# Kernel optimization log

Measured on AMD Instinct MI355X. Metric: run time of the kernel, lower is better.

The kernel has to match this reference:

```python
import jax, jax.numpy as jnp
import numpy as np

B = 8192
I = 1024
H = 1024


def _xavier(key, out_dim, in_dim):
    limit = float(np.sqrt(6.0 / (in_dim + out_dim)))
    return jax.random.uniform(key, (out_dim, in_dim), jnp.float32, -limit, limit)


def setup_inputs() -> dict:
    key = jax.random.key(0)
    ks = jax.random.split(key, 16)
    inp = {
        "x": jax.random.normal(ks[0], (B, I), jnp.float32),
        "h_prev": jax.random.normal(ks[1], (B, H), jnp.float32),
        "c_prev": jax.random.normal(ks[2], (B, H), jnp.float32),
        # input->hidden weights (hidden_size, input_size), hidden->hidden (hidden_size, hidden_size)
        "Wxi": _xavier(ks[3], H, I), "Whi": _xavier(ks[4], H, H),
        "Wxf": _xavier(ks[5], H, I), "Whf": _xavier(ks[6], H, H),
        "Wxc": _xavier(ks[7], H, I), "Whc": _xavier(ks[8], H, H),
        "Wxo": _xavier(ks[9], H, I), "Who": _xavier(ks[10], H, H),
        "bxi": jnp.zeros((H,), jnp.float32), "bhi": jnp.zeros((H,), jnp.float32),
        # forget-gate biases initialized to ones per _init_weights
        "bxf": jnp.ones((H,), jnp.float32), "bhf": jnp.ones((H,), jnp.float32),
        "bxc": jnp.zeros((H,), jnp.float32), "bhc": jnp.zeros((H,), jnp.float32),
        "bxo": jnp.zeros((H,), jnp.float32), "bho": jnp.zeros((H,), jnp.float32),
    }
    return inp


def reference(x, h_prev, c_prev,
              Wxi, Whi, Wxf, Whf, Wxc, Whc, Wxo, Who,
              bxi, bhi, bxf, bhf, bxc, bhc, bxo, bho):
    # Fuse the 8 small linears into two GEMMs: stack along the output (gate) axis.
    Wx = jnp.concatenate([Wxi, Wxf, Wxc, Wxo], axis=0)   # (4H, I)
    Wh = jnp.concatenate([Whi, Whf, Whc, Who], axis=0)   # (4H, H)
    bx = jnp.concatenate([bxi, bxf, bxc, bxo], axis=0)    # (4H,)
    bh = jnp.concatenate([bhi, bhf, bhc, bho], axis=0)    # (4H,)
    gates = x @ Wx.T + h_prev @ Wh.T + (bx + bh)           # (B, 4H)
    zi, zf, zc, zo = jnp.split(gates, 4, axis=1)
    i = jax.nn.sigmoid(zi)
    f = jax.nn.sigmoid(zf)
    g = jnp.tanh(zc)
    o = jax.nn.sigmoid(zo)
    c_new = f * c_prev + i * g
    h_new = o * jnp.tanh(c_new)
    return (h_new, c_new)
```

## Files before the change

kernel.cpp:

```cpp
#include <hip/hip_runtime.h>
#include <hip/hip_bf16.h>
#include <stdint.h>


#define B_DIM 8192
#define I_DIM 1024
#define H_DIM 1024
#define K_DIM 2048
#define N_DIM 4096
#define NKT   32

typedef short bf16x8 __attribute__((ext_vector_type(8)));
typedef float f32x4 __attribute__((ext_vector_type(4)));

__device__ __forceinline__ unsigned short f2bf(float f) {
  unsigned int u = __float_as_uint(f);
  u += 0x7FFFu + ((u >> 16) & 1u);
  return (unsigned short)(u >> 16);
}

__global__ void pack_A_kernel(const float* __restrict__ x,
                              const float* __restrict__ h,
                              unsigned short* __restrict__ outA) {
  const int total = B_DIM * K_DIM / 8;
  for (int idx = blockIdx.x * blockDim.x + threadIdx.x; idx < total;
       idx += gridDim.x * blockDim.x) {
    int row = idx >> 8;
    int col = (idx & 255) * 8;
    const float* src = (col < I_DIM) ? (x + (size_t)row * I_DIM + col)
                                     : (h + (size_t)row * H_DIM + (col - I_DIM));
    const float4* s4 = (const float4*)src;
    float4 v0 = s4[0], v1 = s4[1];
    bf16x8 o;
    o[0] = f2bf(v0.x); o[1] = f2bf(v0.y); o[2] = f2bf(v0.z); o[3] = f2bf(v0.w);
    o[4] = f2bf(v1.x); o[5] = f2bf(v1.y); o[6] = f2bf(v1.z); o[7] = f2bf(v1.w);
    *(bf16x8*)(outA + (size_t)idx * 8) = o;
  }
}

__global__ void pack_B_kernel(const float* __restrict__ Wxi, const float* __restrict__ Whi,
                              const float* __restrict__ Wxf, const float* __restrict__ Whf,
                              const float* __restrict__ Wxc, const float* __restrict__ Whc,
                              const float* __restrict__ Wxo, const float* __restrict__ Who,
                              unsigned short* __restrict__ outB) {
  const int total = N_DIM * K_DIM / 8;
  for (int idx = blockIdx.x * blockDim.x + threadIdx.x; idx < total;
       idx += gridDim.x * blockDim.x) {
    int r = idx >> 8;
    int k = (idx & 255) * 8;
    int g = (r >> 4) & 3;
    int h = ((r >> 6) << 4) | (r & 15);
    const float* base;
    if (k < I_DIM) {
      base = (g == 0) ? Wxi : (g == 1) ? Wxf : (g == 2) ? Wxc : Wxo;
      base += (size_t)h * I_DIM + k;
    } else {
      base = (g == 0) ? Whi : (g == 1) ? Whf : (g == 2) ? Whc : Who;
      base += (size_t)h * H_DIM + (k - I_DIM);
    }
    const float4* s4 = (const float4*)base;
    float4 v0 = s4[0], v1 = s4[1];
    bf16x8 o;
    o[0] = f2bf(v0.x); o[1] = f2bf(v0.y); o[2] = f2bf(v0.z); o[3] = f2bf(v0.w);
    o[4] = f2bf(v1.x); o[5] = f2bf(v1.y); o[6] = f2bf(v1.z); o[7] = f2bf(v1.w);
    *(bf16x8*)(outB + (size_t)idx * 8) = o;
  }
}


#define STAGE(gptr, slotoff, ktile) do {                                          \
    int _ktc = (ktile) < NKT ? (ktile) : (NKT - 1);                               \
    const unsigned short* _g = (gptr) + (size_t)_ktc * 64;                        \
    __builtin_amdgcn_global_load_lds(                                             \
        (const __attribute__((address_space(1))) void*)_g,                        \
        (__attribute__((address_space(3))) void*)(lds + (slotoff) + wid * 1024),  \
        16, 0, 0);                                                                \
    __builtin_amdgcn_global_load_lds(                                             \
        (const __attribute__((address_space(1))) void*)(_g + (size_t)64 * K_DIM), \
        (__attribute__((address_space(3))) void*)(lds + (slotoff) + 8192 + wid * 1024), \
        16, 0, 0);                                                                \
  } while (0)

#define MFMAQ(Q, AR)                                                              \
  _Pragma("unroll") for (int mq = 0; mq < 2; ++mq)                                \
  _Pragma("unroll") for (int nn = 0; nn < 4; ++nn)                                \
  _Pragma("unroll") for (int kk = 0; kk < 2; ++kk)                                \
    acc[(Q)*2 + mq][nn] = __builtin_amdgcn_mfma_f32_16x16x32_bf16(                \
        AR[mq][kk], Bf[nn][kk], acc[(Q)*2 + mq][nn], 0, 0, 0)

#define RD_A(DST, Q)                                                              \
  _Pragma("unroll") for (int mq = 0; mq < 2; ++mq) {                              \
    DST[mq][0] = *(const bf16x8*)(ldsAr + _bo + (Q) * 4096 + mq * 2048 + rd0);    \
    DST[mq][1] = *(const bf16x8*)(ldsAr + _bo + (Q) * 4096 + mq * 2048 + rd1); }

#define KTILE(BUF, KT) do {                                                       \
    const int _bo = (BUF) * 32768;                                                \
    const int _bo1 = ((BUF) ^ 1) * 32768;                                         \
         \
    _Pragma("unroll") for (int nn = 0; nn < 4; ++nn) {                            \
      Bf[nn][0] = *(const bf16x8*)(ldsBr + _bo + nn * 2048 + rd0);                \
      Bf[nn][1] = *(const bf16x8*)(ldsBr + _bo + nn * 2048 + rd1); }              \
    RD_A(AX, 0);                                                                  \
    RD_A(AY, 1);                                                                  \
    STAGE(gA0p, _bo1, (KT) + 1);                                                  \
    __builtin_amdgcn_s_barrier();                                                 \
    __builtin_amdgcn_s_setprio(1);                                                \
    MFMAQ(0, AX);                                                                 \
    __builtin_amdgcn_s_setprio(0);                                                \
    __builtin_amdgcn_s_barrier();                                                 \
          \
    RD_A(AX, 2);                                                                  \
    STAGE(gA1p, _bo1 + 16384, (KT) + 1);                                          \
    __builtin_amdgcn_s_barrier();                                                 \
    __builtin_amdgcn_s_setprio(1);                                                \
    MFMAQ(1, AY);                                                                 \
    __builtin_amdgcn_s_setprio(0);                                                \
    __builtin_amdgcn_s_barrier();                                                 \
        \
    RD_A(AY, 3);                                                                  \
    STAGE(gB0p, 65536 + _bo, (KT) + 2);                                           \
    __builtin_amdgcn_s_barrier();                                                 \
    __builtin_amdgcn_s_setprio(1);                                                \
    MFMAQ(2, AX);                                                                 \
    __builtin_amdgcn_s_setprio(0);                                                \
    __builtin_amdgcn_s_barrier();                                                 \
                                                   \
    STAGE(gB1p, 65536 + _bo + 16384, (KT) + 2);                                   \
    __builtin_amdgcn_s_barrier();                                                 \
    __builtin_amdgcn_s_setprio(1);                                                \
    MFMAQ(3, AY);                                                                 \
    __builtin_amdgcn_s_setprio(0);                                                \
    asm volatile("s_waitcnt vmcnt(4)" ::: "memory");                              \
    __builtin_amdgcn_s_barrier();                                                 \
  } while (0)

__launch_bounds__(512, 2)
__global__ void lstm_gemm_kernel(const unsigned short* __restrict__ A,
                                 const unsigned short* __restrict__ Bp,
                                 const float* __restrict__ c_prev,
                                 const float* __restrict__ bxi, const float* __restrict__ bhi,
                                 const float* __restrict__ bxf, const float* __restrict__ bhf,
                                 const float* __restrict__ bxc, const float* __restrict__ bhc,
                                 const float* __restrict__ bxo, const float* __restrict__ bho,
                                 float* __restrict__ out) {
  __shared__ __align__(16) char lds[131072];

  const int nwg = gridDim.x;
  int bid = blockIdx.x;
  int q = nwg >> 3;
  int wg = (bid & 7) * q + (bid >> 3);
  int bm = wg >> 4;
  int bn = wg & 15;

  int tid = threadIdx.x;
  int lane = tid & 63;
  int wid = tid >> 6;
  int wm = wid >> 2;
  int wn = wid & 3;

  int srow = lane >> 3;
  int schunk = (lane & 7) ^ srow;
  const unsigned short* gA0p = A  + (size_t)(bm * 256 + wid * 8 + srow) * K_DIM + schunk * 8;
  const unsigned short* gA1p = gA0p + (size_t)128 * K_DIM;
  const unsigned short* gB0p = Bp + (size_t)(bn * 256 + wid * 8 + srow) * K_DIM + schunk * 8;
  const unsigned short* gB1p = gB0p + (size_t)128 * K_DIM;

  int c15 = lane & 15;
  int kl = lane >> 4;
  const char* ldsAr = lds + wm * 16384 + c15 * 128;
  const char* ldsBr = lds + 65536 + (wn >> 1) * 16384 + ((wn & 1) * 64 + c15) * 128;
  int rd0 = ((kl) ^ (lane & 7)) << 4;
  int rd1 = ((4 | kl) ^ (lane & 7)) << 4;

  f32x4 acc[8][4];
  f32x4 zero = {0.f, 0.f, 0.f, 0.f};
#pragma unroll
  for (int m = 0; m < 8; ++m)
#pragma unroll
    for (int n = 0; n < 4; ++n) acc[m][n] = zero;

  bf16x8 Bf[4][2];
  bf16x8 AX[2][2];
  bf16x8 AY[2][2];

  STAGE(gA0p, 0, 0);
  STAGE(gA1p, 16384, 0);
  STAGE(gB0p, 65536, 0);
  STAGE(gB1p, 65536 + 16384, 0);
  STAGE(gB0p, 65536 + 32768, 1);
  STAGE(gB1p, 65536 + 32768 + 16384, 1);
  asm volatile("s_waitcnt vmcnt(4)" ::: "memory");
  __builtin_amdgcn_s_barrier();

#pragma unroll 1
  for (int kt = 0; kt < NKT; kt += 2) {
    KTILE(0, kt);
    KTILE(1, kt + 1);
  }

  int h = (bn * 4 + wn) * 16 + c15;
  float bi = bxi[h] + bhi[h];
  float bf_ = bxf[h] + bhf[h];
  float bc = bxc[h] + bhc[h];
  float bo = bxo[h] + bho[h];
  int row0 = bm * 256 + wm * 128 + kl * 4;
#pragma unroll
  for (int mi = 0; mi < 8; ++mi) {
#pragma unroll
    for (int j = 0; j < 4; ++j) {
      int r = row0 + mi * 16 + j;
      size_t off = (size_t)r * H_DIM + h;
      float zi = acc[mi][0][j] + bi;
      float zf = acc[mi][1][j] + bf_;
      float zc = acc[mi][2][j] + bc;
      float zo = acc[mi][3][j] + bo;
      float ig = 1.f / (1.f + __expf(-zi));
      float fg = 1.f / (1.f + __expf(-zf));
      float e2 = __expf(-2.f * zc);
      float gg = (1.f - e2) / (1.f + e2);
      float og = 1.f / (1.f + __expf(-zo));
      float cp = c_prev[off];
      float cn = fg * cp + ig * gg;
      float e2c = __expf(-2.f * cn);
      float th = (1.f - e2c) / (1.f + e2c);
      out[off] = og * th;
      out[(size_t)B_DIM * H_DIM + off] = cn;
    }
  }
}

extern "C" void kernel_launch(void* const* d_in, const int* in_sizes, int n_in,
                              void* d_out, int out_size, void* d_ws, size_t ws_size,
                              hipStream_t stream) {
  const float* x      = (const float*)d_in[0];
  const float* h_prev = (const float*)d_in[1];
  const float* c_prev = (const float*)d_in[2];
  const float* Wxi = (const float*)d_in[3];
  const float* Whi = (const float*)d_in[4];
  const float* Wxf = (const float*)d_in[5];
  const float* Whf = (const float*)d_in[6];
  const float* Wxc = (const float*)d_in[7];
  const float* Whc = (const float*)d_in[8];
  const float* Wxo = (const float*)d_in[9];
  const float* Who = (const float*)d_in[10];
  const float* bxi = (const float*)d_in[11];
  const float* bhi = (const float*)d_in[12];
  const float* bxf = (const float*)d_in[13];
  const float* bhf = (const float*)d_in[14];
  const float* bxc = (const float*)d_in[15];
  const float* bhc = (const float*)d_in[16];
  const float* bxo = (const float*)d_in[17];
  const float* bho = (const float*)d_in[18];

  unsigned short* Abf = (unsigned short*)d_ws;
  unsigned short* Bbf = (unsigned short*)((char*)d_ws + (size_t)B_DIM * K_DIM * 2);

  pack_A_kernel<<<2048, 256, 0, stream>>>(x, h_prev, Abf);
  pack_B_kernel<<<1024, 256, 0, stream>>>(Wxi, Whi, Wxf, Whf, Wxc, Whc, Wxo, Who, Bbf);
  lstm_gemm_kernel<<<512, 512, 0, stream>>>(Abf, Bbf, c_prev,
      bxi, bhi, bxf, bhf, bxc, bhc, bxo, bho, (float*)d_out);
}
```

Measured before the change: 160.7 us.

## Restructure K-tile pipeline to split K halves and prefetch A two tiles ahead

Reorganizes each K-tile into four MFMA phases that loop over M-halves and K-halves, with register double-buffering (AQa/AQb, BHa/BHb). LDS reads for the next phase now run after the current MFMAs, and the first fragments of the next tile are loaded at the end of the current one. A tiles are now staged two iterations ahead like B, and the prologue preloads both buffers. The aim is to cut barriers per tile and overlap LDS reads with MFMA. The cost is tighter hazard reasoning about buffer reuse and waitcnt accounting.

```diff
diff --git a/kernel.cpp b/kernel.cpp
--- a/kernel.cpp
+++ b/kernel.cpp
@@ -81,56 +81,53 @@
         16, 0, 0);                                                                \
   } while (0)
 
-#define MFMAQ(Q, AR)                                                              \
-  _Pragma("unroll") for (int mq = 0; mq < 2; ++mq)                                \
+#define MFMAP(MH, AR, BR)                                                         \
+  _Pragma("unroll") for (int mf = 0; mf < 4; ++mf)                                \
   _Pragma("unroll") for (int nn = 0; nn < 4; ++nn)                                \
-  _Pragma("unroll") for (int kk = 0; kk < 2; ++kk)                                \
-    acc[(Q)*2 + mq][nn] = __builtin_amdgcn_mfma_f32_16x16x32_bf16(                \
-        AR[mq][kk], Bf[nn][kk], acc[(Q)*2 + mq][nn], 0, 0, 0)
-
-#define RD_A(DST, Q)                                                              \
-  _Pragma("unroll") for (int mq = 0; mq < 2; ++mq) {                              \
-    DST[mq][0] = *(const bf16x8*)(ldsAr + _bo + (Q) * 4096 + mq * 2048 + rd0);    \
-    DST[mq][1] = *(const bf16x8*)(ldsAr + _bo + (Q) * 4096 + mq * 2048 + rd1); }
+    acc[(MH)*4 + mf][nn] = __builtin_amdgcn_mfma_f32_16x16x32_bf16(               \
+        AR[mf], BR[nn], acc[(MH)*4 + mf][nn], 0, 0, 0)
+
+#define RD_AQ(DST, MH, KOFF, BO)                                                  \
+  _Pragma("unroll") for (int mf = 0; mf < 4; ++mf)                                \
+    DST[mf] = *(const bf16x8*)(ldsAr + (BO) + (MH)*8192 + mf * 2048 + (KOFF));
+
+#define RD_BH(DST, KOFF, BO)                                                      \
+  _Pragma("unroll") for (int nn = 0; nn < 4; ++nn)                                \
+    DST[nn] = *(const bf16x8*)(ldsBr + (BO) + nn * 2048 + (KOFF));
 
 #define KTILE(BUF, KT) do {                                                       \
     const int _bo = (BUF) * 32768;                                                \
     const int _bo1 = ((BUF) ^ 1) * 32768;                                         \
-         \
-    _Pragma("unroll") for (int nn = 0; nn < 4; ++nn) {                            \
-      Bf[nn][0] = *(const bf16x8*)(ldsBr + _bo + nn * 2048 + rd0);                \
-      Bf[nn][1] = *(const bf16x8*)(ldsBr + _bo + nn * 2048 + rd1); }              \
-    RD_A(AX, 0);                                                                  \
-    RD_A(AY, 1);                                                                  \
-    STAGE(gA0p, _bo1, (KT) + 1);                                                  \
-    __builtin_amdgcn_s_barrier();                                                 \
-    __builtin_amdgcn_s_setprio(1);                                                \
-    MFMAQ(0, AX);                                                                 \
-    __builtin_amdgcn_s_setprio(0);                                                \
-    __builtin_amdgcn_s_barrier();                                                 \
-          \
-    RD_A(AX, 2);                                                                  \
-    STAGE(gA1p, _bo1 + 16384, (KT) + 1);                                          \
-    __builtin_amdgcn_s_barrier();                                                 \
-    __builtin_amdgcn_s_setprio(1);                                                \
-    MFMAQ(1, AY);                                                                 \
-    __builtin_amdgcn_s_setprio(0);                                                \
-    __builtin_amdgcn_s_barrier();                                                 \
-        \
-    RD_A(AY, 3);                                                                  \
+                                                                          \
+    __builtin_amdgcn_s_setprio(1);                                                \
+    MFMAP(0, AQa, BHa);                                                           \
+    __builtin_amdgcn_s_setprio(0);                                                \
+    RD_AQ(AQb, 1, rd0, _bo);                                                      \
+    __builtin_amdgcn_s_barrier();                                                 \
+                                                                          \
+    __builtin_amdgcn_s_setprio(1);                                                \
+    MFMAP(1, AQb, BHa);                                                           \
+    __builtin_amdgcn_s_setprio(0);                                                \
+    RD_BH(BHb, rd1, _bo);                                                         \
+    RD_AQ(AQa, 0, rd1, _bo);                                                      \
+    __builtin_amdgcn_s_barrier();                                                 \
+                                                                          \
+    __builtin_amdgcn_s_setprio(1);                                                \
+    MFMAP(0, AQa, BHb);                                                           \
+    __builtin_amdgcn_s_setprio(0);                                                \
+    RD_AQ(AQb, 1, rd1, _bo);                                                      \
     STAGE(gB0p, 65536 + _bo, (KT) + 2);                                           \
-    __builtin_amdgcn_s_barrier();                                                 \
-    __builtin_amdgcn_s_setprio(1);                                                \
-    MFMAQ(2, AX);                                                                 \
-    __builtin_amdgcn_s_setprio(0);                                                \
-    __builtin_amdgcn_s_barrier();                                                 \
-                                                   \
     STAGE(gB1p, 65536 + _bo + 16384, (KT) + 2);                                   \
-    __builtin_amdgcn_s_barrier();                                                 \
-    __builtin_amdgcn_s_setprio(1);                                                \
-    MFMAQ(3, AY);                                                                 \
-    __builtin_amdgcn_s_setprio(0);                                                \
     asm volatile("s_waitcnt vmcnt(4)" ::: "memory");                              \
+    __builtin_amdgcn_s_barrier();                                                 \
+                                                                          \
+    __builtin_amdgcn_s_setprio(1);                                                \
+    MFMAP(1, AQb, BHb);                                                           \
+    __builtin_amdgcn_s_setprio(0);                                                \
+    RD_AQ(AQa, 0, rd0, _bo1);                                                     \
+    RD_BH(BHa, rd0, _bo1);                                                        \
+    STAGE(gA0p, _bo, (KT) + 2);                                                   \
+    STAGE(gA1p, _bo + 16384, (KT) + 2);                                           \
     __builtin_amdgcn_s_barrier();                                                 \
   } while (0)
 
@@ -179,18 +176,21 @@
 #pragma unroll
     for (int n = 0; n < 4; ++n) acc[m][n] = zero;
 
-  bf16x8 Bf[4][2];
-  bf16x8 AX[2][2];
-  bf16x8 AY[2][2];
+  bf16x8 AQa[4], AQb[4];
+  bf16x8 BHa[4], BHb[4];
 
   STAGE(gA0p, 0, 0);
   STAGE(gA1p, 16384, 0);
   STAGE(gB0p, 65536, 0);
   STAGE(gB1p, 65536 + 16384, 0);
+  STAGE(gA0p, 32768, 1);
+  STAGE(gA1p, 32768 + 16384, 1);
   STAGE(gB0p, 65536 + 32768, 1);
   STAGE(gB1p, 65536 + 32768 + 16384, 1);
-  asm volatile("s_waitcnt vmcnt(4)" ::: "memory");
+  asm volatile("s_waitcnt vmcnt(8)" ::: "memory");
   __builtin_amdgcn_s_barrier();
+  RD_AQ(AQa, 0, rd0, 0);
+  RD_BH(BHa, rd0, 0);
 
 #pragma unroll 1
   for (int kt = 0; kt < NKT; kt += 2) {
```

After: 153.6 us. -4.4%, faster.
